# Kernel tuning notes

Measured on AMD Instinct MI355X. Metric: run time of the kernel, lower is better.

Reference implementation:

```python
import jax, jax.numpy as jnp
import numpy as np
import math

ALPHA = 2.0  # spikingjelly surrogate.ATan default alpha
TAU = 2.0
MEM_DECAY = math.exp(-1.0 / TAU)
ADAPT_STRENGTH = 0.1
TARGET_RATE = 0.02
THR_MIN = 0.5
N_HEAD = 4

@jax.custom_vjp
def spike_fn(x):
    # Heaviside forward, ATan surrogate backward
    return (x >= 0.0).astype(x.dtype)

def _spike_fwd(x):
    return spike_fn(x), x

def _spike_bwd(x, g):
    return (g * (ALPHA / 2.0) / (1.0 + (jnp.pi / 2.0 * ALPHA * x) ** 2),)

spike_fn.defvjp(_spike_fwd, _spike_bwd)

def lif_step(x, v_mem, thr):
    # thr is a buffer in torch (updated under no_grad): no grad flows to it
    thr_c = jax.lax.stop_gradient(thr)
    v_pot = v_mem * MEM_DECAY + x
    spike = spike_fn(v_pot - thr_c)
    v_new = v_pot * (1.0 - jax.lax.stop_gradient(spike))
    err = jax.lax.stop_gradient(jnp.mean(spike)) - TARGET_RATE
    thr_new = jnp.maximum(thr_c + ADAPT_STRENGTH * err, THR_MIN)
    return spike, v_new, thr_new

def setup_inputs() -> dict:
    key = jax.random.key(0)
    ks = jax.random.split(key, 10)
    B, T, S, D, DS = 8, 16, 256, 512, 64
    x = jax.random.normal(ks[0], (B, T, S, D), jnp.float32)
    A = jax.random.normal(ks[1], (DS, DS), jnp.float32)
    C = jax.random.normal(ks[2], (D, DS), jnp.float32)
    s = 1.0 / math.sqrt(DS)
    Wq = jax.random.uniform(ks[3], (DS, DS), jnp.float32, -s, s)
    bq = jax.random.uniform(ks[4], (DS,), jnp.float32, -s, s)
    sd = 1.0 / math.sqrt(D)
    Wkv = jax.random.uniform(ks[5], (2 * DS, D), jnp.float32, -sd, sd)
    bkv = jax.random.uniform(ks[6], (2 * DS,), jnp.float32, -sd, sd)
    Wo = jax.random.uniform(ks[7], (DS, DS), jnp.float32, -s, s)
    bo = jax.random.uniform(ks[8], (DS,), jnp.float32, -s, s)
    thr_s0 = jnp.full((DS,), 1.0, jnp.float32)
    thr_o0 = jnp.full((D,), 1.0, jnp.float32)
    return {"x": x, "A": A, "C": C, "Wq": Wq, "bq": bq, "Wkv": Wkv,
            "bkv": bkv, "Wo": Wo, "bo": bo, "thr_s0": thr_s0, "thr_o0": thr_o0}

def reference(x, A, C, Wq, bq, Wkv, bkv, Wo, bo, thr_s0, thr_o0):
    B, T, S, D = x.shape
    DS = A.shape[0]
    H = N_HEAD
    dh = DS // H
    N = B * S
    scale = 1.0 / math.sqrt(dh)
    h0 = jnp.zeros((B, S, DS), x.dtype)
    sv0 = jnp.zeros((B, S, DS), x.dtype)
    ov0 = jnp.zeros((B, S, D), x.dtype)

    def step(carry, x_t):
        h, sv, ov, ts, to = carry
        state_transition = h @ A.T                              # (B,S,DS)
        q = (h @ Wq.T + bq).reshape(N, H, dh).transpose(1, 0, 2)   # (H,N,dh)
        kv = x_t @ Wkv.T + bkv                                  # (B,S,2*DS)
        k = kv[..., :DS].reshape(N, H, dh).transpose(1, 0, 2)   # (H,N,dh)
        v = kv[..., DS:].reshape(N, H, dh).transpose(1, 0, 2)   # (H,N,dh)
        scores = jnp.einsum('hnd,hmd->hnm', q, k) * scale       # (H,N,N)
        w = jax.nn.softmax(scores, axis=-1)
        att = jnp.einsum('hnm,hmd->hnd', w, v)                  # (H,N,dh)
        att = att.transpose(1, 0, 2).reshape(B, S, DS)
        state_update = state_transition + att @ Wo.T + bo
        h2, sv2, ts2 = lif_step(state_update, sv, ts)
        output_potential = h2 @ C.T                             # (B,S,D)
        out, ov2, to2 = lif_step(output_potential, ov, to)
        return (h2, sv2, ov2, ts2, to2), out

    _, outs = jax.lax.scan(step, (h0, sv0, ov0, thr_s0, thr_o0),
                           jnp.moveaxis(x, 1, 0))               # outs: (T,B,S,D)
    return jnp.moveaxis(outs, 0, 1)                             # (B,T,S,D)
```

## Files before the change

kernel.cpp:

```cpp
#include <hip/hip_runtime.h>
#include <math.h>


#define NTOK   2048
#define TSTEPS 16
#define NSPLIT 32

#define MEMDECAY ((float)0.6065306597126334)
#define SCALE    0.25f
#define LOG2E    1.4426950408889634f

#define OFF_KV   ((size_t)0)
#define OFF_PACC ((size_t)4194304)
#define OFF_OV   ((size_t)8388608)
#define OFF_H    ((size_t)9437184)
#define OFF_SV   ((size_t)9568256)
#define OFF_Q    ((size_t)9699328)
#define OFF_PM   ((size_t)9830400)
#define OFF_PL   ((size_t)10092544)
#define OFF_CT   ((size_t)10354688)
#define OFF_CNT  ((size_t)10387456)
#define OFF_WT   ((size_t)10387488)
#define OFF_HM   ((size_t)10453024)

__global__ __launch_bounds__(256) void init_kernel(const float* __restrict__ bq,
                                                   const float* __restrict__ C,
                                                   const float* __restrict__ Wkv,
                                                   float* __restrict__ ws) {
  int i = blockIdx.x * 256 + threadIdx.x;
  if (i < 327680) {
    float4 z = {0.f, 0.f, 0.f, 0.f};
    ((float4*)(ws + OFF_OV))[i] = z;
    return;
  }
  i -= 327680;
  if (i < 131072) { ws[OFF_Q + i] = bq[i & 63]; return; }
  i -= 131072;
  if (i < 32768) {
    int k = i >> 9, c = i & 511;
    ws[OFF_CT + i] = C[c * 64 + k];
    return;
  }
  i -= 32768;
  if (i < 65536) {
    int k = i >> 7, o = i & 127;
    ws[OFF_WT + i] = Wkv[o * 512 + k];
    return;
  }
  i -= 65536;
  if (i < 32) { ((int*)(ws + OFF_CNT))[i] = 0; return; }
  i -= 32;
  if (i < 1024) {
    float4 z = {0.f, 0.f, 0.f, 0.f};
    ((float4*)(ws + OFF_HM))[i] = z;
  }
}

__global__ __launch_bounds__(256) void kv_gemm_kernel(const float* __restrict__ x,
                                                      const float* __restrict__ wkt,
                                                      const float* __restrict__ bkv,
                                                      float* __restrict__ ws) {
  __shared__ float xs[64 * 68];
  __shared__ float wt[64 * 136];
  const int tid = threadIdx.x;
  const int mbase = blockIdx.x * 64;
  const int rg = tid >> 4;
  const int cg = tid & 15;

  float acc[4][8];
#pragma unroll
  for (int i = 0; i < 4; ++i)
#pragma unroll
    for (int j = 0; j < 8; ++j) acc[i][j] = 0.f;

  for (int kt = 0; kt < 8; ++kt) {
    const int kb = kt * 64;
#pragma unroll
    for (int p = 0; p < 4; ++p) {
      int e = tid + p * 256;
      int r = e >> 4, kq = e & 15;
      int row = mbase + r;
      int t_ = row >> 11, n = row & 2047;
      int b = n >> 8, s = n & 255;
      float4 v = *(const float4*)(x + (size_t)((b * 16 + t_) * 256 + s) * 512 + kb + kq * 4);
      *(float4*)(xs + r * 68 + kq * 4) = v;
    }
#pragma unroll
    for (int p = 0; p < 8; ++p) {
      int e = tid + p * 256;
      int k = e >> 5, cq = e & 31;
      float4 v = *(const float4*)(wkt + (size_t)(kb + k) * 128 + cq * 4);
      *(float4*)(wt + k * 136 + cq * 4) = v;
    }
    __syncthreads();
#pragma unroll 2
    for (int kq = 0; kq < 16; ++kq) {
      float4 a0 = *(const float4*)(xs + (rg * 4 + 0) * 68 + kq * 4);
      float4 a1 = *(const float4*)(xs + (rg * 4 + 1) * 68 + kq * 4);
      float4 a2 = *(const float4*)(xs + (rg * 4 + 2) * 68 + kq * 4);
      float4 a3 = *(const float4*)(xs + (rg * 4 + 3) * 68 + kq * 4);
      const float* ap[4] = {(const float*)&a0, (const float*)&a1,
                            (const float*)&a2, (const float*)&a3};
#pragma unroll
      for (int kk = 0; kk < 4; ++kk) {
        const float* wp = wt + (kq * 4 + kk) * 136;
        float4 b0 = *(const float4*)(wp + cg * 4);
        float4 b1 = *(const float4*)(wp + 64 + cg * 4);
#pragma unroll
        for (int i = 0; i < 4; ++i) {
          float av = ap[i][kk];
          acc[i][0] += av * b0.x; acc[i][1] += av * b0.y;
          acc[i][2] += av * b0.z; acc[i][3] += av * b0.w;
          acc[i][4] += av * b1.x; acc[i][5] += av * b1.y;
          acc[i][6] += av * b1.z; acc[i][7] += av * b1.w;
        }
      }
    }
    __syncthreads();
  }
  float4 bb0 = *(const float4*)(bkv + cg * 4);
  float4 bb1 = *(const float4*)(bkv + 64 + cg * 4);
  float* kvout = ws + OFF_KV;
#pragma unroll
  for (int i = 0; i < 4; ++i) {
    float* op = kvout + (size_t)(mbase + rg * 4 + i) * 128;
    float4 v0; v0.x = acc[i][0] + bb0.x; v0.y = acc[i][1] + bb0.y;
    v0.z = acc[i][2] + bb0.z; v0.w = acc[i][3] + bb0.w;
    float4 v1; v1.x = acc[i][4] + bb1.x; v1.y = acc[i][5] + bb1.y;
    v1.z = acc[i][6] + bb1.z; v1.w = acc[i][7] + bb1.w;
    *(float4*)(op + cg * 4) = v0;
    *(float4*)(op + 64 + cg * 4) = v1;
  }
}

__device__ __forceinline__ void attp_body(int blk, int tid, int t,
                                          const float* __restrict__ kvbase,
                                          const float* __restrict__ qbuf,
                                          float* __restrict__ pm,
                                          float* __restrict__ pl,
                                          float* __restrict__ pacc,
                                          float* smem) {
  const int head = blk & 3;
  const int qt = (blk >> 2) & 3;
  const int sp = blk >> 4;
  float* kl = smem;
  float* vl = smem + 1024;
  const float* kvt = kvbase + (size_t)t * NTOK * 128;
  {
    int key = tid >> 2, dq = tid & 3;
    const float* base = kvt + (size_t)(sp * 64 + key) * 128 + head * 16;
    float4 kk = ((const float4*)base)[dq];
    float4 vv = ((const float4*)(base + 64))[dq];
    ((float4*)kl)[key * 4 + dq] = kk;
    ((float4*)vl)[key * 4 + dq] = vv;
  }
  const int i0 = qt * 512 + tid;
  const int i1 = i0 + 256;
  float q0[16], q1[16];
  {
    const float4* qp0 = (const float4*)(qbuf + (size_t)i0 * 64 + head * 16);
    const float4* qp1 = (const float4*)(qbuf + (size_t)i1 * 64 + head * 16);
#pragma unroll
    for (int r = 0; r < 4; ++r) {
      float4 a = qp0[r];
      q0[4 * r] = a.x; q0[4 * r + 1] = a.y; q0[4 * r + 2] = a.z; q0[4 * r + 3] = a.w;
      float4 b = qp1[r];
      q1[4 * r] = b.x; q1[4 * r + 1] = b.y; q1[4 * r + 2] = b.z; q1[4 * r + 3] = b.w;
    }
  }
  __syncthreads();
  float m0 = -INFINITY, l0 = 0.f, m1 = -INFINITY, l1 = 0.f;
  float acc0[16], acc1[16];
#pragma unroll
  for (int d = 0; d < 16; ++d) { acc0[d] = 0.f; acc1[d] = 0.f; }

#pragma unroll
  for (int ch = 0; ch < 4; ++ch) {
    float sc0[16], sc1[16];
#pragma unroll
    for (int j = 0; j < 16; ++j) {
      const float* kp = kl + (ch * 16 + j) * 16;
      float s0 = 0.f, s1 = 0.f;
#pragma unroll
      for (int d = 0; d < 16; ++d) { float kv_ = kp[d]; s0 += q0[d] * kv_; s1 += q1[d] * kv_; }
      sc0[j] = s0 * SCALE; sc1[j] = s1 * SCALE;
    }
    float mb0 = sc0[0], mb1 = sc1[0];
#pragma unroll
    for (int j = 1; j < 16; ++j) { mb0 = fmaxf(mb0, sc0[j]); mb1 = fmaxf(mb1, sc1[j]); }
    float mn0 = fmaxf(m0, mb0), mn1 = fmaxf(m1, mb1);
    float r0 = exp2f((m0 - mn0) * LOG2E), r1 = exp2f((m1 - mn1) * LOG2E);
    l0 *= r0; l1 *= r1;
#pragma unroll
    for (int d = 0; d < 16; ++d) { acc0[d] *= r0; acc1[d] *= r1; }
#pragma unroll
    for (int j = 0; j < 16; ++j) {
      float w0 = exp2f((sc0[j] - mn0) * LOG2E), w1 = exp2f((sc1[j] - mn1) * LOG2E);
      l0 += w0; l1 += w1; sc0[j] = w0; sc1[j] = w1;
    }
#pragma unroll
    for (int j = 0; j < 16; ++j) {
      const float* vp = vl + (ch * 16 + j) * 16;
      float w0 = sc0[j], w1 = sc1[j];
#pragma unroll
      for (int d = 0; d < 16; ++d) { float vv = vp[d]; acc0[d] += w0 * vv; acc1[d] += w1 * vv; }
    }
    m0 = mn0; m1 = mn1;
  }
  const int pbase = (head * NSPLIT + sp) * NTOK;
  pm[pbase + i0] = m0; pm[pbase + i1] = m1;
  pl[pbase + i0] = l0; pl[pbase + i1] = l1;
  float4* pa0 = (float4*)(pacc + (size_t)(pbase + i0) * 16);
  float4* pa1 = (float4*)(pacc + (size_t)(pbase + i1) * 16);
#pragma unroll
  for (int r = 0; r < 4; ++r) {
    float4 v0; v0.x = acc0[4 * r]; v0.y = acc0[4 * r + 1]; v0.z = acc0[4 * r + 2]; v0.w = acc0[4 * r + 3];
    pa0[r] = v0;
    float4 v1; v1.x = acc1[4 * r]; v1.y = acc1[4 * r + 1]; v1.z = acc1[4 * r + 2]; v1.w = acc1[4 * r + 3];
    pa1[r] = v1;
  }
}

__global__ __launch_bounds__(256) void attp_kernel(int t, float* __restrict__ ws) {
  __shared__ float smem[2048];
  attp_body(blockIdx.x, threadIdx.x, t, ws + OFF_KV, ws + OFF_Q,
            ws + OFF_PM, ws + OFF_PL, ws + OFF_PACC, smem);
}

__global__ __launch_bounds__(256) void combine_lifs_kernel(
    int t, const float* __restrict__ A, const float* __restrict__ Wq,
    const float* __restrict__ bq, const float* __restrict__ Wo,
    const float* __restrict__ bo, const float* __restrict__ thr_s0,
    float* __restrict__ ws) {
  __shared__ float As[64 * 68], Wqs[64 * 68], Wos[64 * 68];
  __shared__ float att_s[4][64];
  __shared__ int scnt;
  const int tid = threadIdx.x;
#pragma unroll
  for (int p = 0; p < 4; ++p) {
    int e = tid + p * 256;
    int c = e >> 4, kq = e & 15;
    *(float4*)(As + c * 68 + kq * 4)  = *(const float4*)(A + c * 64 + kq * 4);
    *(float4*)(Wqs + c * 68 + kq * 4) = *(const float4*)(Wq + c * 64 + kq * 4);
    *(float4*)(Wos + c * 68 + kq * 4) = *(const float4*)(Wo + c * 64 + kq * 4);
  }
  if (tid == 0) scnt = 0;

  const float* pm = ws + OFF_PM;
  const float* pl = ws + OFF_PL;
  const float* pacc = ws + OFF_PACC;
  float* sv = ws + OFF_SV;
  float* qb = ws + OFF_Q;
  int* cnt = (int*)(ws + OFF_CNT);
  unsigned long long* hmask = (unsigned long long*)(ws + OFF_HM);

  const int lane = tid & 63, w = tid >> 6;
  const int n = blockIdx.x * 4 + w;
  const int head = lane >> 4, d = lane & 15;
  const int pb = head * NSPLIT * NTOK + n;

  float mstar = -INFINITY;
  for (int s = 0; s < NSPLIT; ++s) mstar = fmaxf(mstar, pm[pb + s * NTOK]);
  float lst = 0.f, av = 0.f;
  for (int s = 0; s < NSPLIT; ++s) {
    float e = exp2f((pm[pb + s * NTOK] - mstar) * LOG2E);
    lst += e * pl[pb + s * NTOK];
    av += e * pacc[(size_t)(pb + s * NTOK) * 16 + d];
  }
  att_s[w][lane] = av / lst;
  unsigned long long hm = hmask[n];
  __syncthreads();

  float st = 0.f;
  {
    unsigned long long m = hm;
    while (m) {
      int k = __builtin_ctzll(m);
      m &= m - 1;
      st += As[lane * 68 + k];
    }
  }
  const float* Wor = Wos + lane * 68;
  float wo = 0.f;
#pragma unroll
  for (int kq = 0; kq < 16; ++kq) {
    float4 wb = *(const float4*)(Wor + kq * 4);
    float4 ab = *(const float4*)(&att_s[w][kq * 4]);
    wo += ab.x * wb.x; wo += ab.y * wb.y; wo += ab.z * wb.z; wo += ab.w * wb.w;
  }
  float su = st + wo + bo[lane];

  float thr = thr_s0[0];
  const float inv = 1.0f / 131072.0f;
  for (int i = 0; i < t; ++i) {
    float mean = (float)cnt[i] * inv;
    thr = fmaxf(thr + 0.1f * (mean - 0.02f), 0.5f);
  }
  float svo = sv[n * 64 + lane];
  float vpot = svo * MEMDECAY + su;
  float spk = (vpot >= thr) ? 1.f : 0.f;
  sv[n * 64 + lane] = vpot * (1.f - spk);
  unsigned long long sm = __ballot(spk > 0.5f);

  float qv = 0.f;
  {
    unsigned long long m = sm;
    while (m) {
      int k = __builtin_ctzll(m);
      m &= m - 1;
      qv += Wqs[lane * 68 + k];
    }
  }
  qb[n * 64 + lane] = qv + bq[lane];

  if (lane == 0) {
    hmask[n] = sm;
    atomicAdd(&scnt, __popcll(sm));
  }
  __syncthreads();
  if (tid == 0) atomicAdd(&cnt[t], scnt);
}

__global__ __launch_bounds__(256) void fused_out_attp_kernel(
    int t, const float* __restrict__ thr_o0, float* __restrict__ out,
    float* __restrict__ ws) {
  __shared__ float smem[2048];
  __shared__ int scnt;
  const int blk = blockIdx.x;
  if (blk >= 256) {
    attp_body(blk - 256, threadIdx.x, t + 1, ws + OFF_KV, ws + OFF_Q,
              ws + OFF_PM, ws + OFF_PL, ws + OFF_PACC, smem);
    return;
  }
  const int tid = threadIdx.x;
  const int nt = blk >> 3;
  const int ct = blk & 7;
  const float* Ct = ws + OFF_CT;
  float* ov = ws + OFF_OV;
  int* cnt = (int*)(ws + OFF_CNT);
  const unsigned long long* hmask = (const unsigned long long*)(ws + OFF_HM);

  if (tid == 0) scnt = 0;
  __syncthreads();

  const int tr = tid >> 4, tc = tid & 15;
  float thr = thr_o0[0];
  const float inv = 1.0f / 1048576.0f;
  for (int i = 0; i < t; ++i) {
    float mean = (float)cnt[16 + i] * inv;
    thr = fmaxf(thr + 0.1f * (mean - 0.02f), 0.5f);
  }

  int mycount = 0;
#pragma unroll
  for (int i = 0; i < 4; ++i) {
    int n = nt * 64 + tr + i * 16;
    size_t coff = (size_t)ct * 64 + tc * 4;
    float a0 = 0.f, a1 = 0.f, a2 = 0.f, a3 = 0.f;
    unsigned long long m = hmask[n];
    while (m) {
      int k = __builtin_ctzll(m);
      m &= m - 1;
      float4 c = *(const float4*)(Ct + (size_t)k * 512 + coff);
      a0 += c.x; a1 += c.y; a2 += c.z; a3 += c.w;
    }
    int b = n >> 8, s = n & 255;
    float* ovp = ov + (size_t)n * 512 + coff;
    float* outp = out + ((size_t)(b * 16 + t) * 256 + s) * 512 + coff;
    float4 o = *(float4*)ovp;
    float v0 = o.x * MEMDECAY + a0;
    float v1 = o.y * MEMDECAY + a1;
    float v2 = o.z * MEMDECAY + a2;
    float v3 = o.w * MEMDECAY + a3;
    float s0 = (v0 >= thr) ? 1.f : 0.f;
    float s1 = (v1 >= thr) ? 1.f : 0.f;
    float s2 = (v2 >= thr) ? 1.f : 0.f;
    float s3 = (v3 >= thr) ? 1.f : 0.f;
    float4 sp; sp.x = s0; sp.y = s1; sp.z = s2; sp.w = s3;
    *(float4*)outp = sp;
    float4 nv; nv.x = v0 * (1.f - s0); nv.y = v1 * (1.f - s1);
    nv.z = v2 * (1.f - s2); nv.w = v3 * (1.f - s3);
    *(float4*)ovp = nv;
    mycount += (int)(s0 + s1 + s2 + s3);
  }
  atomicAdd(&scnt, mycount);
  __syncthreads();
  if (tid == 0) atomicAdd(&cnt[16 + t], scnt);
}

extern "C" void kernel_launch(void* const* d_in, const int* in_sizes, int n_in,
                              void* d_out, int out_size, void* d_ws, size_t ws_size,
                              hipStream_t stream) {
  const float* x    = (const float*)d_in[0];
  const float* A    = (const float*)d_in[1];
  const float* C    = (const float*)d_in[2];
  const float* Wq   = (const float*)d_in[3];
  const float* bq   = (const float*)d_in[4];
  const float* Wkv  = (const float*)d_in[5];
  const float* bkv  = (const float*)d_in[6];
  const float* Wo   = (const float*)d_in[7];
  const float* bo   = (const float*)d_in[8];
  const float* th_s = (const float*)d_in[9];
  const float* th_o = (const float*)d_in[10];
  float* out = (float*)d_out;
  float* ws = (float*)d_ws;

  init_kernel<<<dim3(2181), dim3(256), 0, stream>>>(bq, C, Wkv, ws);
  kv_gemm_kernel<<<dim3(512), dim3(256), 0, stream>>>(x, ws + OFF_WT, bkv, ws);
  attp_kernel<<<dim3(512), dim3(256), 0, stream>>>(0, ws);
  for (int t = 0; t < TSTEPS; ++t) {
    combine_lifs_kernel<<<dim3(512), dim3(256), 0, stream>>>(t, A, Wq, bq, Wo, bo, th_s, ws);
    int g = (t < TSTEPS - 1) ? 768 : 256;
    fused_out_attp_kernel<<<dim3(g), dim3(256), 0, stream>>>(t, th_o, out, ws);
  }
}
```

Before: 910.3 us.

## Fuse output LIF into combine kernel, run attention partials separately

The output-layer spike accumulation and LIF update move into the combine kernel, using the freshly computed state spike mask directly, with each lane covering 8 output columns. The attention-partial work for the next step becomes its own launch instead of sharing a grid with the output LIF. A and Wq are now read from global/L1 instead of being staged in shared memory, and the split-softmax loops are unrolled. This trades less LDS staging and one fewer cross-kernel handoff of the mask for less overlap between output LIF and attention partials, and for per-lane scattered Ct reads.

```diff
diff --git a/kernel.cpp b/kernel.cpp
--- a/kernel.cpp
+++ b/kernel.cpp
@@ -13,7 +13,6 @@
 #define OFF_KV   ((size_t)0)
 #define OFF_PACC ((size_t)4194304)
 #define OFF_OV   ((size_t)8388608)
-#define OFF_H    ((size_t)9437184)
 #define OFF_SV   ((size_t)9568256)
 #define OFF_Q    ((size_t)9699328)
 #define OFF_PM   ((size_t)9830400)
@@ -227,24 +226,23 @@
             ws + OFF_PM, ws + OFF_PL, ws + OFF_PACC, smem);
 }
 
-__global__ __launch_bounds__(256) void combine_lifs_kernel(
+__global__ __launch_bounds__(256) void combine_out_kernel(
     int t, const float* __restrict__ A, const float* __restrict__ Wq,
     const float* __restrict__ bq, const float* __restrict__ Wo,
     const float* __restrict__ bo, const float* __restrict__ thr_s0,
+    const float* __restrict__ thr_o0, float* __restrict__ out,
     float* __restrict__ ws) {
-  __shared__ float As[64 * 68], Wqs[64 * 68], Wos[64 * 68];
+  __shared__ float Wos[64 * 68];
   __shared__ float att_s[4][64];
-  __shared__ int scnt;
+  __shared__ int scnt, ocnt;
   const int tid = threadIdx.x;
 #pragma unroll
   for (int p = 0; p < 4; ++p) {
     int e = tid + p * 256;
     int c = e >> 4, kq = e & 15;
-    *(float4*)(As + c * 68 + kq * 4)  = *(const float4*)(A + c * 64 + kq * 4);
-    *(float4*)(Wqs + c * 68 + kq * 4) = *(const float4*)(Wq + c * 64 + kq * 4);
     *(float4*)(Wos + c * 68 + kq * 4) = *(const float4*)(Wo + c * 64 + kq * 4);
   }
-  if (tid == 0) scnt = 0;
+  if (tid == 0) { scnt = 0; ocnt = 0; }
 
   const float* pm = ws + OFF_PM;
   const float* pl = ws + OFF_PL;
@@ -260,8 +258,10 @@
   const int pb = head * NSPLIT * NTOK + n;
 
   float mstar = -INFINITY;
+#pragma unroll
   for (int s = 0; s < NSPLIT; ++s) mstar = fmaxf(mstar, pm[pb + s * NTOK]);
   float lst = 0.f, av = 0.f;
+#pragma unroll
   for (int s = 0; s < NSPLIT; ++s) {
     float e = exp2f((pm[pb + s * NTOK] - mstar) * LOG2E);
     lst += e * pl[pb + s * NTOK];
@@ -269,6 +269,7 @@
   }
   att_s[w][lane] = av / lst;
   unsigned long long hm = hmask[n];
+
   __syncthreads();
 
   float st = 0.f;
@@ -277,7 +278,7 @@
     while (m) {
       int k = __builtin_ctzll(m);
       m &= m - 1;
-      st += As[lane * 68 + k];
+      st += A[lane * 64 + k];
     }
   }
   const float* Wor = Wos + lane * 68;
@@ -308,7 +309,7 @@
     while (m) {
       int k = __builtin_ctzll(m);
       m &= m - 1;
-      qv += Wqs[lane * 68 + k];
+      qv += Wq[lane * 64 + k];
     }
   }
   qb[n * 64 + lane] = qv + bq[lane];
@@ -317,65 +318,44 @@
     hmask[n] = sm;
     atomicAdd(&scnt, __popcll(sm));
   }
-  __syncthreads();
-  if (tid == 0) atomicAdd(&cnt[t], scnt);
-}
-
-__global__ __launch_bounds__(256) void fused_out_attp_kernel(
-    int t, const float* __restrict__ thr_o0, float* __restrict__ out,
-    float* __restrict__ ws) {
-  __shared__ float smem[2048];
-  __shared__ int scnt;
-  const int blk = blockIdx.x;
-  if (blk >= 256) {
-    attp_body(blk - 256, threadIdx.x, t + 1, ws + OFF_KV, ws + OFF_Q,
-              ws + OFF_PM, ws + OFF_PL, ws + OFF_PACC, smem);
-    return;
-  }
-  const int tid = threadIdx.x;
-  const int nt = blk >> 3;
-  const int ct = blk & 7;
+
   const float* Ct = ws + OFF_CT;
   float* ov = ws + OFF_OV;
-  int* cnt = (int*)(ws + OFF_CNT);
-  const unsigned long long* hmask = (const unsigned long long*)(ws + OFF_HM);
-
-  if (tid == 0) scnt = 0;
-  __syncthreads();
-
-  const int tr = tid >> 4, tc = tid & 15;
-  float thr = thr_o0[0];
-  const float inv = 1.0f / 1048576.0f;
+  float thro = thr_o0[0];
+  const float invo = 1.0f / 1048576.0f;
   for (int i = 0; i < t; ++i) {
-    float mean = (float)cnt[16 + i] * inv;
-    thr = fmaxf(thr + 0.1f * (mean - 0.02f), 0.5f);
-  }
-
-  int mycount = 0;
-#pragma unroll
-  for (int i = 0; i < 4; ++i) {
-    int n = nt * 64 + tr + i * 16;
-    size_t coff = (size_t)ct * 64 + tc * 4;
-    float a0 = 0.f, a1 = 0.f, a2 = 0.f, a3 = 0.f;
-    unsigned long long m = hmask[n];
+    float mean = (float)cnt[16 + i] * invo;
+    thro = fmaxf(thro + 0.1f * (mean - 0.02f), 0.5f);
+  }
+  const size_t coff = (size_t)lane * 8;
+  float a0 = 0.f, a1 = 0.f, a2 = 0.f, a3 = 0.f;
+  float a4 = 0.f, a5 = 0.f, a6 = 0.f, a7 = 0.f;
+  {
+    unsigned long long m = sm;
     while (m) {
       int k = __builtin_ctzll(m);
       m &= m - 1;
-      float4 c = *(const float4*)(Ct + (size_t)k * 512 + coff);
-      a0 += c.x; a1 += c.y; a2 += c.z; a3 += c.w;
-    }
-    int b = n >> 8, s = n & 255;
-    float* ovp = ov + (size_t)n * 512 + coff;
-    float* outp = out + ((size_t)(b * 16 + t) * 256 + s) * 512 + coff;
+      const float* cp = Ct + (size_t)k * 512 + coff;
+      float4 c0 = *(const float4*)(cp);
+      float4 c1 = *(const float4*)(cp + 4);
+      a0 += c0.x; a1 += c0.y; a2 += c0.z; a3 += c0.w;
+      a4 += c1.x; a5 += c1.y; a6 += c1.z; a7 += c1.w;
+    }
+  }
+  int b = n >> 8, s_ = n & 255;
+  float* ovp = ov + (size_t)n * 512 + coff;
+  float* outp = out + ((size_t)(b * 16 + t) * 256 + s_) * 512 + coff;
+  int mycount = 0;
+  {
     float4 o = *(float4*)ovp;
     float v0 = o.x * MEMDECAY + a0;
     float v1 = o.y * MEMDECAY + a1;
     float v2 = o.z * MEMDECAY + a2;
     float v3 = o.w * MEMDECAY + a3;
-    float s0 = (v0 >= thr) ? 1.f : 0.f;
-    float s1 = (v1 >= thr) ? 1.f : 0.f;
-    float s2 = (v2 >= thr) ? 1.f : 0.f;
-    float s3 = (v3 >= thr) ? 1.f : 0.f;
+    float s0 = (v0 >= thro) ? 1.f : 0.f;
+    float s1 = (v1 >= thro) ? 1.f : 0.f;
+    float s2 = (v2 >= thro) ? 1.f : 0.f;
+    float s3 = (v3 >= thro) ? 1.f : 0.f;
     float4 sp; sp.x = s0; sp.y = s1; sp.z = s2; sp.w = s3;
     *(float4*)outp = sp;
     float4 nv; nv.x = v0 * (1.f - s0); nv.y = v1 * (1.f - s1);
@@ -383,9 +363,29 @@
     *(float4*)ovp = nv;
     mycount += (int)(s0 + s1 + s2 + s3);
   }
-  atomicAdd(&scnt, mycount);
+  {
+    float4 o = *(float4*)(ovp + 4);
+    float v0 = o.x * MEMDECAY + a4;
+    float v1 = o.y * MEMDECAY + a5;
+    float v2 = o.z * MEMDECAY + a6;
+    float v3 = o.w * MEMDECAY + a7;
+    float s0 = (v0 >= thro) ? 1.f : 0.f;
+    float s1 = (v1 >= thro) ? 1.f : 0.f;
+    float s2 = (v2 >= thro) ? 1.f : 0.f;
+    float s3 = (v3 >= thro) ? 1.f : 0.f;
+    float4 sp; sp.x = s0; sp.y = s1; sp.z = s2; sp.w = s3;
+    *(float4*)(outp + 4) = sp;
+    float4 nv; nv.x = v0 * (1.f - s0); nv.y = v1 * (1.f - s1);
+    nv.z = v2 * (1.f - s2); nv.w = v3 * (1.f - s3);
+    *(float4*)(ovp + 4) = nv;
+    mycount += (int)(s0 + s1 + s2 + s3);
+  }
+  atomicAdd(&ocnt, mycount);
   __syncthreads();
-  if (tid == 0) atomicAdd(&cnt[16 + t], scnt);
+  if (tid == 0) {
+    atomicAdd(&cnt[t], scnt);
+    atomicAdd(&cnt[16 + t], ocnt);
+  }
 }
 
 extern "C" void kernel_launch(void* const* d_in, const int* in_sizes, int n_in,
@@ -409,8 +409,9 @@
   kv_gemm_kernel<<<dim3(512), dim3(256), 0, stream>>>(x, ws + OFF_WT, bkv, ws);
   attp_kernel<<<dim3(512), dim3(256), 0, stream>>>(0, ws);
   for (int t = 0; t < TSTEPS; ++t) {
-    combine_lifs_kernel<<<dim3(512), dim3(256), 0, stream>>>(t, A, Wq, bq, Wo, bo, th_s, ws);
-    int g = (t < TSTEPS - 1) ? 768 : 256;
-    fused_out_attp_kernel<<<dim3(g), dim3(256), 0, stream>>>(t, th_o, out, ws);
-  }
-}
+    combine_out_kernel<<<dim3(512), dim3(256), 0, stream>>>(
+        t, A, Wq, bq, Wo, bo, th_s, th_o, out, ws);
+    if (t < TSTEPS - 1)
+      attp_kernel<<<dim3(512), dim3(256), 0, stream>>>(t + 1, ws);
+  }
+}
```

Result: slower. 931.7 us (+2.4%).

## Split attention partial keys across thread groups, four queries per thread, LDS merge

Applied to the files above, without the earlier changes.

Each thread in the partial-attention body now handles four query rows instead of two, and the 64-key chunk is split between two 128-thread groups that each process 32 keys. The two groups' online-softmax states are merged through a new shared-memory buffer before the partials are written. The goal is more reuse of each LDS K/V load across queries, cutting LDS traffic per FLOP. The cost is a larger shared-memory footprint (48KB), higher register pressure from four accumulators of 16 floats, and an extra barrier plus merge step.

```diff
diff --git a/kernel.cpp b/kernel.cpp
--- a/kernel.cpp
+++ b/kernel.cpp
@@ -13,7 +13,6 @@
 #define OFF_KV   ((size_t)0)
 #define OFF_PACC ((size_t)4194304)
 #define OFF_OV   ((size_t)8388608)
-#define OFF_H    ((size_t)9437184)
 #define OFF_SV   ((size_t)9568256)
 #define OFF_Q    ((size_t)9699328)
 #define OFF_PM   ((size_t)9830400)
@@ -22,6 +21,8 @@
 #define OFF_CNT  ((size_t)10387456)
 #define OFF_WT   ((size_t)10387488)
 #define OFF_HM   ((size_t)10453024)
+
+#define ATTP_SMEM 12288
 
 __global__ __launch_bounds__(256) void init_kernel(const float* __restrict__ bq,
                                                    const float* __restrict__ C,
@@ -145,84 +146,125 @@
   const int sp = blk >> 4;
   float* kl = smem;
   float* vl = smem + 1024;
+  float* ab = smem + 2048;
   const float* kvt = kvbase + (size_t)t * NTOK * 128;
   {
     int key = tid >> 2, dq = tid & 3;
     const float* base = kvt + (size_t)(sp * 64 + key) * 128 + head * 16;
-    float4 kk = ((const float4*)base)[dq];
-    float4 vv = ((const float4*)(base + 64))[dq];
-    ((float4*)kl)[key * 4 + dq] = kk;
-    ((float4*)vl)[key * 4 + dq] = vv;
-  }
-  const int i0 = qt * 512 + tid;
-  const int i1 = i0 + 256;
-  float q0[16], q1[16];
-  {
-    const float4* qp0 = (const float4*)(qbuf + (size_t)i0 * 64 + head * 16);
-    const float4* qp1 = (const float4*)(qbuf + (size_t)i1 * 64 + head * 16);
+    ((float4*)kl)[key * 4 + dq] = ((const float4*)base)[dq];
+    ((float4*)vl)[key * 4 + dq] = ((const float4*)(base + 64))[dq];
+  }
+  const int grp = tid >> 7;
+  const int lt = tid & 127;
+  float q[4][16];
+#pragma unroll
+  for (int r = 0; r < 4; ++r) {
+    const float4* qp = (const float4*)(qbuf + (size_t)(qt * 512 + lt + r * 128) * 64 + head * 16);
+#pragma unroll
+    for (int x = 0; x < 4; ++x) {
+      float4 a = qp[x];
+      q[r][4 * x] = a.x; q[r][4 * x + 1] = a.y;
+      q[r][4 * x + 2] = a.z; q[r][4 * x + 3] = a.w;
+    }
+  }
+  __syncthreads();
+  float m[4], l[4], acc[4][16];
+#pragma unroll
+  for (int r = 0; r < 4; ++r) {
+    m[r] = -INFINITY; l[r] = 0.f;
+#pragma unroll
+    for (int d = 0; d < 16; ++d) acc[r][d] = 0.f;
+  }
+  const int kb = grp * 32;
+#pragma unroll
+  for (int ch = 0; ch < 4; ++ch) {
+    float sc[4][8];
+#pragma unroll
+    for (int j = 0; j < 8; ++j) {
+      const float* kp = kl + (kb + ch * 8 + j) * 16;
+      float s0 = 0.f, s1 = 0.f, s2 = 0.f, s3 = 0.f;
+#pragma unroll
+      for (int d = 0; d < 16; ++d) {
+        float kvv = kp[d];
+        s0 += q[0][d] * kvv; s1 += q[1][d] * kvv;
+        s2 += q[2][d] * kvv; s3 += q[3][d] * kvv;
+      }
+      sc[0][j] = s0 * SCALE; sc[1][j] = s1 * SCALE;
+      sc[2][j] = s2 * SCALE; sc[3][j] = s3 * SCALE;
+    }
 #pragma unroll
     for (int r = 0; r < 4; ++r) {
-      float4 a = qp0[r];
-      q0[4 * r] = a.x; q0[4 * r + 1] = a.y; q0[4 * r + 2] = a.z; q0[4 * r + 3] = a.w;
-      float4 b = qp1[r];
-      q1[4 * r] = b.x; q1[4 * r + 1] = b.y; q1[4 * r + 2] = b.z; q1[4 * r + 3] = b.w;
-    }
-  }
-  __syncthreads();
-  float m0 = -INFINITY, l0 = 0.f, m1 = -INFINITY, l1 = 0.f;
-  float acc0[16], acc1[16];
-#pragma unroll
-  for (int d = 0; d < 16; ++d) { acc0[d] = 0.f; acc1[d] = 0.f; }
-
-#pragma unroll
-  for (int ch = 0; ch < 4; ++ch) {
-    float sc0[16], sc1[16];
-#pragma unroll
-    for (int j = 0; j < 16; ++j) {
-      const float* kp = kl + (ch * 16 + j) * 16;
-      float s0 = 0.f, s1 = 0.f;
-#pragma unroll
-      for (int d = 0; d < 16; ++d) { float kv_ = kp[d]; s0 += q0[d] * kv_; s1 += q1[d] * kv_; }
-      sc0[j] = s0 * SCALE; sc1[j] = s1 * SCALE;
-    }
-    float mb0 = sc0[0], mb1 = sc1[0];
-#pragma unroll
-    for (int j = 1; j < 16; ++j) { mb0 = fmaxf(mb0, sc0[j]); mb1 = fmaxf(mb1, sc1[j]); }
-    float mn0 = fmaxf(m0, mb0), mn1 = fmaxf(m1, mb1);
-    float r0 = exp2f((m0 - mn0) * LOG2E), r1 = exp2f((m1 - mn1) * LOG2E);
-    l0 *= r0; l1 *= r1;
-#pragma unroll
-    for (int d = 0; d < 16; ++d) { acc0[d] *= r0; acc1[d] *= r1; }
-#pragma unroll
-    for (int j = 0; j < 16; ++j) {
-      float w0 = exp2f((sc0[j] - mn0) * LOG2E), w1 = exp2f((sc1[j] - mn1) * LOG2E);
-      l0 += w0; l1 += w1; sc0[j] = w0; sc1[j] = w1;
-    }
-#pragma unroll
-    for (int j = 0; j < 16; ++j) {
-      const float* vp = vl + (ch * 16 + j) * 16;
-      float w0 = sc0[j], w1 = sc1[j];
-#pragma unroll
-      for (int d = 0; d < 16; ++d) { float vv = vp[d]; acc0[d] += w0 * vv; acc1[d] += w1 * vv; }
-    }
-    m0 = mn0; m1 = mn1;
-  }
-  const int pbase = (head * NSPLIT + sp) * NTOK;
-  pm[pbase + i0] = m0; pm[pbase + i1] = m1;
-  pl[pbase + i0] = l0; pl[pbase + i1] = l1;
-  float4* pa0 = (float4*)(pacc + (size_t)(pbase + i0) * 16);
-  float4* pa1 = (float4*)(pacc + (size_t)(pbase + i1) * 16);
-#pragma unroll
-  for (int r = 0; r < 4; ++r) {
-    float4 v0; v0.x = acc0[4 * r]; v0.y = acc0[4 * r + 1]; v0.z = acc0[4 * r + 2]; v0.w = acc0[4 * r + 3];
-    pa0[r] = v0;
-    float4 v1; v1.x = acc1[4 * r]; v1.y = acc1[4 * r + 1]; v1.z = acc1[4 * r + 2]; v1.w = acc1[4 * r + 3];
-    pa1[r] = v1;
+      float mbv = sc[r][0];
+#pragma unroll
+      for (int j = 1; j < 8; ++j) mbv = fmaxf(mbv, sc[r][j]);
+      float mn = fmaxf(m[r], mbv);
+      float rr = exp2f((m[r] - mn) * LOG2E);
+      l[r] *= rr;
+#pragma unroll
+      for (int d = 0; d < 16; ++d) acc[r][d] *= rr;
+#pragma unroll
+      for (int j = 0; j < 8; ++j) {
+        float w = exp2f((sc[r][j] - mn) * LOG2E);
+        l[r] += w; sc[r][j] = w;
+      }
+      m[r] = mn;
+    }
+#pragma unroll
+    for (int j = 0; j < 8; ++j) {
+      const float* vp = vl + (kb + ch * 8 + j) * 16;
+#pragma unroll
+      for (int d = 0; d < 16; ++d) {
+        float vv = vp[d];
+        acc[0][d] += sc[0][j] * vv; acc[1][d] += sc[1][j] * vv;
+        acc[2][d] += sc[2][j] * vv; acc[3][d] += sc[3][j] * vv;
+      }
+    }
+  }
+  if (grp == 1) {
+#pragma unroll
+    for (int r = 0; r < 4; ++r) {
+      int qi = lt + r * 128;
+      float* row = ab + qi * 20;
+#pragma unroll
+      for (int x = 0; x < 4; ++x) {
+        float4 v; v.x = acc[r][4 * x]; v.y = acc[r][4 * x + 1];
+        v.z = acc[r][4 * x + 2]; v.w = acc[r][4 * x + 3];
+        *(float4*)(row + x * 4) = v;
+      }
+      row[16] = m[r]; row[17] = l[r];
+    }
+  }
+  __syncthreads();
+  if (grp == 0) {
+    const int pbase = (head * NSPLIT + sp) * NTOK;
+#pragma unroll
+    for (int r = 0; r < 4; ++r) {
+      int qi = lt + r * 128;
+      const float* row = ab + qi * 20;
+      float m1 = row[16], l1 = row[17];
+      float mn = fmaxf(m[r], m1);
+      float r0 = exp2f((m[r] - mn) * LOG2E);
+      float r1 = exp2f((m1 - mn) * LOG2E);
+      int i = qt * 512 + qi;
+      pm[pbase + i] = mn;
+      pl[pbase + i] = l[r] * r0 + l1 * r1;
+      float4* pa = (float4*)(pacc + (size_t)(pbase + i) * 16);
+#pragma unroll
+      for (int x = 0; x < 4; ++x) {
+        float4 a1 = *(const float4*)(row + x * 4);
+        float4 v;
+        v.x = acc[r][4 * x] * r0 + a1.x * r1;
+        v.y = acc[r][4 * x + 1] * r0 + a1.y * r1;
+        v.z = acc[r][4 * x + 2] * r0 + a1.z * r1;
+        v.w = acc[r][4 * x + 3] * r0 + a1.w * r1;
+        pa[x] = v;
+      }
+    }
   }
 }
 
 __global__ __launch_bounds__(256) void attp_kernel(int t, float* __restrict__ ws) {
-  __shared__ float smem[2048];
+  __shared__ float smem[ATTP_SMEM];
   attp_body(blockIdx.x, threadIdx.x, t, ws + OFF_KV, ws + OFF_Q,
             ws + OFF_PM, ws + OFF_PL, ws + OFF_PACC, smem);
 }
@@ -324,7 +366,7 @@
 __global__ __launch_bounds__(256) void fused_out_attp_kernel(
     int t, const float* __restrict__ thr_o0, float* __restrict__ out,
     float* __restrict__ ws) {
-  __shared__ float smem[2048];
+  __shared__ float smem[ATTP_SMEM];
   __shared__ int scnt;
   const int blk = blockIdx.x;
   if (blk >= 256) {
```

Result: slower. 1.166 ms (+28.1%).

## Drop LDS staging and read weights and K/V directly from global memory

Applied to the files above, without the earlier changes.

Removes the shared-memory staging of Wkv tiles in the KV GEMM, of K/V blocks in the attention partial kernel, and of A/Wq in the combine kernel. Those operands are now loaded straight from global memory, relying on caches and wave-uniform addresses for broadcast. This removes LDS traffic and some barriers and lowers shared-memory use, which may raise occupancy. The cost is more global/cache loads per FMA, most of all in the GEMM inner loop, where every thread re-reads the weight rows.

```diff
diff --git a/kernel.cpp b/kernel.cpp
--- a/kernel.cpp
+++ b/kernel.cpp
@@ -13,7 +13,6 @@
 #define OFF_KV   ((size_t)0)
 #define OFF_PACC ((size_t)4194304)
 #define OFF_OV   ((size_t)8388608)
-#define OFF_H    ((size_t)9437184)
 #define OFF_SV   ((size_t)9568256)
 #define OFF_Q    ((size_t)9699328)
 #define OFF_PM   ((size_t)9830400)
@@ -61,7 +60,6 @@
                                                       const float* __restrict__ bkv,
                                                       float* __restrict__ ws) {
   __shared__ float xs[64 * 68];
-  __shared__ float wt[64 * 136];
   const int tid = threadIdx.x;
   const int mbase = blockIdx.x * 64;
   const int rg = tid >> 4;
@@ -84,13 +82,6 @@
       int b = n >> 8, s = n & 255;
       float4 v = *(const float4*)(x + (size_t)((b * 16 + t_) * 256 + s) * 512 + kb + kq * 4);
       *(float4*)(xs + r * 68 + kq * 4) = v;
-    }
-#pragma unroll
-    for (int p = 0; p < 8; ++p) {
-      int e = tid + p * 256;
-      int k = e >> 5, cq = e & 31;
-      float4 v = *(const float4*)(wkt + (size_t)(kb + k) * 128 + cq * 4);
-      *(float4*)(wt + k * 136 + cq * 4) = v;
     }
     __syncthreads();
 #pragma unroll 2
@@ -103,7 +94,7 @@
                             (const float*)&a2, (const float*)&a3};
 #pragma unroll
       for (int kk = 0; kk < 4; ++kk) {
-        const float* wp = wt + (kq * 4 + kk) * 136;
+        const float* wp = wkt + (size_t)(kb + kq * 4 + kk) * 128;
         float4 b0 = *(const float4*)(wp + cg * 4);
         float4 b1 = *(const float4*)(wp + 64 + cg * 4);
 #pragma unroll
@@ -138,22 +129,12 @@
                                           const float* __restrict__ qbuf,
                                           float* __restrict__ pm,
                                           float* __restrict__ pl,
-                                          float* __restrict__ pacc,
-                                          float* smem) {
+                                          float* __restrict__ pacc) {
   const int head = blk & 3;
   const int qt = (blk >> 2) & 3;
   const int sp = blk >> 4;
-  float* kl = smem;
-  float* vl = smem + 1024;
   const float* kvt = kvbase + (size_t)t * NTOK * 128;
-  {
-    int key = tid >> 2, dq = tid & 3;
-    const float* base = kvt + (size_t)(sp * 64 + key) * 128 + head * 16;
-    float4 kk = ((const float4*)base)[dq];
-    float4 vv = ((const float4*)(base + 64))[dq];
-    ((float4*)kl)[key * 4 + dq] = kk;
-    ((float4*)vl)[key * 4 + dq] = vv;
-  }
+  const float* kbase = kvt + (size_t)(sp * 64) * 128 + head * 16;
   const int i0 = qt * 512 + tid;
   const int i1 = i0 + 256;
   float q0[16], q1[16];
@@ -168,7 +149,6 @@
       q1[4 * r] = b.x; q1[4 * r + 1] = b.y; q1[4 * r + 2] = b.z; q1[4 * r + 3] = b.w;
     }
   }
-  __syncthreads();
   float m0 = -INFINITY, l0 = 0.f, m1 = -INFINITY, l1 = 0.f;
   float acc0[16], acc1[16];
 #pragma unroll
@@ -179,10 +159,27 @@
     float sc0[16], sc1[16];
 #pragma unroll
     for (int j = 0; j < 16; ++j) {
-      const float* kp = kl + (ch * 16 + j) * 16;
+      const float4* kp = (const float4*)(kbase + (size_t)(ch * 16 + j) * 128);
+      float4 k0 = kp[0], k1 = kp[1], k2 = kp[2], k3 = kp[3];
+      const float* kf = (const float*)&k0;
       float s0 = 0.f, s1 = 0.f;
-#pragma unroll
-      for (int d = 0; d < 16; ++d) { float kv_ = kp[d]; s0 += q0[d] * kv_; s1 += q1[d] * kv_; }
+      s0 += q0[0] * k0.x;  s1 += q1[0] * k0.x;
+      s0 += q0[1] * k0.y;  s1 += q1[1] * k0.y;
+      s0 += q0[2] * k0.z;  s1 += q1[2] * k0.z;
+      s0 += q0[3] * k0.w;  s1 += q1[3] * k0.w;
+      s0 += q0[4] * k1.x;  s1 += q1[4] * k1.x;
+      s0 += q0[5] * k1.y;  s1 += q1[5] * k1.y;
+      s0 += q0[6] * k1.z;  s1 += q1[6] * k1.z;
+      s0 += q0[7] * k1.w;  s1 += q1[7] * k1.w;
+      s0 += q0[8] * k2.x;  s1 += q1[8] * k2.x;
+      s0 += q0[9] * k2.y;  s1 += q1[9] * k2.y;
+      s0 += q0[10] * k2.z; s1 += q1[10] * k2.z;
+      s0 += q0[11] * k2.w; s1 += q1[11] * k2.w;
+      s0 += q0[12] * k3.x; s1 += q1[12] * k3.x;
+      s0 += q0[13] * k3.y; s1 += q1[13] * k3.y;
+      s0 += q0[14] * k3.z; s1 += q1[14] * k3.z;
+      s0 += q0[15] * k3.w; s1 += q1[15] * k3.w;
+      (void)kf;
       sc0[j] = s0 * SCALE; sc1[j] = s1 * SCALE;
     }
     float mb0 = sc0[0], mb1 = sc1[0];
@@ -200,10 +197,25 @@
     }
 #pragma unroll
     for (int j = 0; j < 16; ++j) {
-      const float* vp = vl + (ch * 16 + j) * 16;
+      const float4* vp = (const float4*)(kbase + (size_t)(ch * 16 + j) * 128 + 64);
+      float4 v0 = vp[0], v1 = vp[1], v2 = vp[2], v3 = vp[3];
       float w0 = sc0[j], w1 = sc1[j];
-#pragma unroll
-      for (int d = 0; d < 16; ++d) { float vv = vp[d]; acc0[d] += w0 * vv; acc1[d] += w1 * vv; }
+      acc0[0] += w0 * v0.x;  acc1[0] += w1 * v0.x;
+      acc0[1] += w0 * v0.y;  acc1[1] += w1 * v0.y;
+      acc0[2] += w0 * v0.z;  acc1[2] += w1 * v0.z;
+      acc0[3] += w0 * v0.w;  acc1[3] += w1 * v0.w;
+      acc0[4] += w0 * v1.x;  acc1[4] += w1 * v1.x;
+      acc0[5] += w0 * v1.y;  acc1[5] += w1 * v1.y;
+      acc0[6] += w0 * v1.z;  acc1[6] += w1 * v1.z;
+      acc0[7] += w0 * v1.w;  acc1[7] += w1 * v1.w;
+      acc0[8] += w0 * v2.x;  acc1[8] += w1 * v2.x;
+      acc0[9] += w0 * v2.y;  acc1[9] += w1 * v2.y;
+      acc0[10] += w0 * v2.z; acc1[10] += w1 * v2.z;
+      acc0[11] += w0 * v2.w; acc1[11] += w1 * v2.w;
+      acc0[12] += w0 * v3.x; acc1[12] += w1 * v3.x;
+      acc0[13] += w0 * v3.y; acc1[13] += w1 * v3.y;
+      acc0[14] += w0 * v3.z; acc1[14] += w1 * v3.z;
+      acc0[15] += w0 * v3.w; acc1[15] += w1 * v3.w;
     }
     m0 = mn0; m1 = mn1;
   }
@@ -222,9 +234,8 @@
 }
 
 __global__ __launch_bounds__(256) void attp_kernel(int t, float* __restrict__ ws) {
-  __shared__ float smem[2048];
   attp_body(blockIdx.x, threadIdx.x, t, ws + OFF_KV, ws + OFF_Q,
-            ws + OFF_PM, ws + OFF_PL, ws + OFF_PACC, smem);
+            ws + OFF_PM, ws + OFF_PL, ws + OFF_PACC);
 }
 
 __global__ __launch_bounds__(256) void combine_lifs_kernel(
@@ -232,7 +243,7 @@
     const float* __restrict__ bq, const float* __restrict__ Wo,
     const float* __restrict__ bo, const float* __restrict__ thr_s0,
     float* __restrict__ ws) {
-  __shared__ float As[64 * 68], Wqs[64 * 68], Wos[64 * 68];
+  __shared__ float Wos[64 * 68];
   __shared__ float att_s[4][64];
   __shared__ int scnt;
   const int tid = threadIdx.x;
@@ -240,8 +251,6 @@
   for (int p = 0; p < 4; ++p) {
     int e = tid + p * 256;
     int c = e >> 4, kq = e & 15;
-    *(float4*)(As + c * 68 + kq * 4)  = *(const float4*)(A + c * 64 + kq * 4);
-    *(float4*)(Wqs + c * 68 + kq * 4) = *(const float4*)(Wq + c * 64 + kq * 4);
     *(float4*)(Wos + c * 68 + kq * 4) = *(const float4*)(Wo + c * 64 + kq * 4);
   }
   if (tid == 0) scnt = 0;
@@ -269,7 +278,6 @@
   }
   att_s[w][lane] = av / lst;
   unsigned long long hm = hmask[n];
-  __syncthreads();
 
   float st = 0.f;
   {
@@ -277,9 +285,11 @@
     while (m) {
       int k = __builtin_ctzll(m);
       m &= m - 1;
-      st += As[lane * 68 + k];
-    }
-  }
+      st += A[lane * 64 + k];
+    }
+  }
+  __syncthreads();
+
   const float* Wor = Wos + lane * 68;
   float wo = 0.f;
 #pragma unroll
@@ -308,7 +318,7 @@
     while (m) {
       int k = __builtin_ctzll(m);
       m &= m - 1;
-      qv += Wqs[lane * 68 + k];
+      qv += Wq[lane * 64 + k];
     }
   }
   qb[n * 64 + lane] = qv + bq[lane];
@@ -324,12 +334,11 @@
 __global__ __launch_bounds__(256) void fused_out_attp_kernel(
     int t, const float* __restrict__ thr_o0, float* __restrict__ out,
     float* __restrict__ ws) {
-  __shared__ float smem[2048];
   __shared__ int scnt;
   const int blk = blockIdx.x;
   if (blk >= 256) {
     attp_body(blk - 256, threadIdx.x, t + 1, ws + OFF_KV, ws + OFF_Q,
-              ws + OFF_PM, ws + OFF_PL, ws + OFF_PACC, smem);
+              ws + OFF_PM, ws + OFF_PL, ws + OFF_PACC);
     return;
   }
   const int tid = threadIdx.x;
```

New measurement: 1.267 ms. 1.39x slower.
